# Performance work log

Measured on AMD Instinct MI355X. Metric: run time of the kernel, lower is better.

## Reference

```python
import jax, jax.numpy as jnp
import numpy as np

B, T, S, C, F = 32, 50, 2048, 8, 32  # batch, time, spatial steps, in-channels, filters
K, STRIDE = 2, 2
DN = ('NWC', 'WIO', 'NWC')


def hard_sigmoid(x):
    # TF-Keras hard_sigmoid: clip(0.2*x + 0.5, 0, 1)
    return jnp.clip(0.2 * x + 0.5, 0.0, 1.0)


def setup_inputs() -> dict:
    key = jax.random.key(0)
    ks = jax.random.split(key, 5)
    x = jax.random.normal(ks[0], (B, T, S, C), jnp.float32)
    kernel = jax.random.normal(ks[1], (K, C, 4 * F), jnp.float32) * 0.05
    rec_kernel = jax.random.normal(ks[2], (K, F, 4 * F), jnp.float32) * 0.05
    bias = jnp.zeros((4 * F,), jnp.float32)
    dense_w = jax.random.normal(ks[3], ((S // STRIDE) * F, 1), jnp.float32) * 0.02
    dense_b = jnp.zeros((1,), jnp.float32)
    return dict(x=x, kernel=kernel, rec_kernel=rec_kernel, bias=bias,
                dense_w=dense_w, dense_b=dense_b)


def reference(x, kernel, rec_kernel, bias, dense_w, dense_b):
    b, t, s, c = x.shape
    f = rec_kernel.shape[1]
    # Input convolution for all timesteps at once (stride 2, SAME padding)
    xc = jax.lax.conv_general_dilated(x.reshape(b * t, s, c), kernel,
                                      (STRIDE,), 'SAME', dimension_numbers=DN)
    xc = xc + bias
    sh = xc.shape[1]  # ceil(s / stride)
    xc = xc.reshape(b, t, sh, 4 * f).transpose(1, 0, 2, 3)  # time-major for scan

    def step(carry, xt):
        h, cst = carry
        hc = jax.lax.conv_general_dilated(h, rec_kernel, (1,), 'SAME',
                                          dimension_numbers=DN)
        z = xt + hc
        zi, zf, zc, zo = jnp.split(z, 4, axis=-1)
        i = hard_sigmoid(zi)
        fg = hard_sigmoid(zf)
        cst = fg * cst + i * jnp.tanh(zc)
        o = hard_sigmoid(zo)
        h = o * jnp.tanh(cst)
        return (h, cst), None

    h0 = jnp.zeros((b, sh, f), x.dtype)
    (h, _), _ = jax.lax.scan(step, (h0, h0), xc)
    # Flatten + Dense(1)
    return h.reshape(b, -1) @ dense_w + dense_b
```

## Files before the change

kernel.cpp:

```cpp
#include <hip/hip_runtime.h>


#define TT 50
#define LTILE 64
#define ROWS 129
#define HSTR 40

typedef __attribute__((ext_vector_type(8))) short short8;
typedef __attribute__((ext_vector_type(4))) float floatx4;

__device__ short8 g_tw0[512];
__device__ short8 g_tw1[512];
__device__ short8 g_txw[512];

__device__ __forceinline__ unsigned short f2b_rne(float f) {
  union { float f; unsigned u; } v; v.f = f;
  unsigned r = v.u + 0x7FFFu + ((v.u >> 16) & 1u);
  return (unsigned short)(r >> 16);
}
__device__ __forceinline__ unsigned short f2b_trunc(float f) {
  union { float f; unsigned u; } v; v.f = f;
  return (unsigned short)(v.u >> 16);
}
__device__ __forceinline__ float hsig(float x) {
  return __builtin_amdgcn_fmed3f(__builtin_fmaf(0.2f, x, 0.5f), 0.0f, 1.0f);
}
__device__ __forceinline__ float ftanh(float x) {
  float e = __expf(2.0f * x);
  return 1.0f - 2.0f * __builtin_amdgcn_rcpf(e + 1.0f);
}

__global__ void prep(const float* __restrict__ ks,
                     const float* __restrict__ rks,
                     const float* __restrict__ bs,
                     float* __restrict__ ws) {
  const int lane = threadIdx.x;
  if (lane < 32) ws[lane] = 0.0f;
  const int q  = lane >> 4;
  const int f0 = lane & 15;
#pragma unroll
  for (int n = 0; n < 8; ++n) {
    const int oc = (n >> 1) * 32 + 2 * f0 + (n & 1);
    short8 th;
#pragma unroll
    for (int j = 0; j < 8; ++j)
      th[j] = (short)f2b_rne(rks[(q * 8 + j) * 128 + oc]);
    g_tw0[n * 64 + lane] = th;
#pragma unroll
    for (int j = 0; j < 8; ++j)
      th[j] = (short)f2b_rne(rks[(32 + q * 8 + j) * 128 + oc]);
    g_tw1[n * 64 + lane] = th;
    short8 tx = {0, 0, 0, 0, 0, 0, 0, 0};
    if (q < 2) {
#pragma unroll
      for (int j = 0; j < 8; ++j)
        tx[j] = (short)f2b_rne(ks[(q * 8 + j) * 128 + oc]);
    } else if (q == 2) {
      tx[0] = (short)f2b_rne(bs[oc]);
    }
    g_txw[n * 64 + lane] = tx;
  }
}

__global__ __launch_bounds__(256, 2)
void convlstm_scan(const float* __restrict__ xs,
                   const float* __restrict__ dws,
                   float* __restrict__ acc_out) {
  __shared__ short hbH[2][ROWS * HSTR];

  const int tid  = threadIdx.x;
  const int b    = blockIdx.x >> 4;
  const int j0   = (blockIdx.x & 15) * LTILE;
  const int wave = tid >> 6;
  const int lane = tid & 63;
  const int q    = lane >> 4;
  const int f0   = lane & 15;

  for (int e = tid; e < ROWS * HSTR; e += 256)
    ((int*)hbH)[e] = 0;

  short8 Bwh0[8], Bwh1[8], Bxw[8];
#pragma unroll
  for (int n = 0; n < 8; ++n) {
    Bwh0[n] = g_tw0[n * 64 + lane];
    Bwh1[n] = g_tw1[n * 64 + lane];
    Bxw[n]  = g_txw[n * 64 + lane];
  }

  short8 axc = {0, 0, 0, 0, 0, 0, 0, 0};
  if (q == 2) axc[0] = (short)0x3F80;

  const floatx4 zero4 = {0.0f, 0.0f, 0.0f, 0.0f};

  float cst[2][8];
#pragma unroll
  for (int s = 0; s < 2; ++s)
#pragma unroll
    for (int i = 0; i < 8; ++i) cst[s][i] = 0.0f;

  floatx4 px0[2], px1[2];
#pragma unroll
  for (int s = 0; s < 2; ++s) {
    const int jr = (wave + 4 * s) * 16 + f0;
    const int jm = min(j0 + jr, 1023);
    const float* xp = xs + (size_t)b * TT * (2048 * 8) +
                      (size_t)(2 * jm + (q & 1)) * 8;
    px0[s] = *(const floatx4*)xp;
    px1[s] = *(const floatx4*)(xp + 4);
  }

  const int maxrows = 1024 - j0;
  float part = 0.0f;
  __syncthreads();

  for (int t = 0; t < TT; ++t) {
    const short* curH = hbH[t & 1];
    short* nxtH = hbH[(t & 1) ^ 1];
    int rows = LTILE + (TT - 1) - t;
    if (rows > maxrows) rows = maxrows;
    const int nmt = (rows + 15) >> 4;
    const int act1 = (wave + 4) < nmt;
    const int last = (t == TT - 1);
    const int tn = last ? t : t + 1;
    const float* xnext = xs + ((size_t)(b * TT + tn)) * (2048 * 8);

    short8 a0h[2], a1h[2];
#pragma unroll
    for (int s = 0; s < 2; ++s) {
      const int jr = (wave + 4 * s) * 16 + f0;
      a0h[s] = *(const short8*)&curH[jr * HSTR + q * 8];
      a1h[s] = *(const short8*)&curH[(jr + 1) * HSTR + q * 8];
    }

    short8 ax[2];
#pragma unroll
    for (int s = 0; s < 2; ++s) {
      ax[s] = axc;
      if (q < 2) {
        floatx4 x0 = px0[s], x1 = px1[s];
#pragma unroll
        for (int jj = 0; jj < 4; ++jj) ax[s][jj] = (short)f2b_trunc(x0[jj]);
#pragma unroll
        for (int jj = 0; jj < 4; ++jj) ax[s][4 + jj] = (short)f2b_trunc(x1[jj]);
      }
    }

#pragma unroll
    for (int s = 0; s < 2; ++s) {
      const int jr = (wave + 4 * s) * 16 + f0;
      const int jm = min(j0 + jr, 1023);
      const float* xp = xnext + (size_t)(2 * jm + (q & 1)) * 8;
      px0[s] = *(const floatx4*)xp;
      px1[s] = *(const floatx4*)(xp + 4);
    }

#pragma unroll
    for (int s = 0; s < 2; ++s) {
      if (s == 1 && !act1) continue;
      const int m = wave + 4 * s;

      floatx4 acc[8];
#pragma unroll
      for (int n = 0; n < 8; ++n)
        acc[n] = __builtin_amdgcn_mfma_f32_16x16x32_bf16(ax[s], Bxw[n], zero4, 0, 0, 0);
#pragma unroll
      for (int n = 0; n < 8; ++n)
        acc[n] = __builtin_amdgcn_mfma_f32_16x16x32_bf16(a0h[s], Bwh0[n], acc[n], 0, 0, 0);
#pragma unroll
      for (int n = 0; n < 8; ++n)
        acc[n] = __builtin_amdgcn_mfma_f32_16x16x32_bf16(a1h[s], Bwh1[n], acc[n], 0, 0, 0);

      const int jw = m * 16 + q * 4;
#pragma unroll
      for (int r = 0; r < 4; ++r) {
        float hv2[2];
#pragma unroll
        for (int p = 0; p < 2; ++p) {
          float zi = acc[0 + p][r], zf = acc[2 + p][r];
          float zc = acc[4 + p][r], zo = acc[6 + p][r];
          float ig = hsig(zi), fg = hsig(zf), og = hsig(zo);
          float cs = cst[s][p * 4 + r];
          float cn = __builtin_fmaf(fg, cs, ig * ftanh(zc));
          cst[s][p * 4 + r] = cn;
          hv2[p] = og * ftanh(cn);
        }
        if (!last) {
          unsigned pk;
          asm("v_cvt_pk_bf16_f32 %0, %1, %2"
              : "=v"(pk) : "v"(hv2[0]), "v"(hv2[1]));
          *(unsigned*)&nxtH[(jw + r) * HSTR + 2 * f0] = pk;
        } else {
          const int di = (j0 + jw + r) * 32 + 2 * f0;
          part = __builtin_fmaf(hv2[0], dws[di],
                 __builtin_fmaf(hv2[1], dws[di + 1], part));
        }
      }
    }
    __syncthreads();
  }

#pragma unroll
  for (int off = 32; off > 0; off >>= 1) part += __shfl_down(part, off);
  if (lane == 0) atomicAdd(&acc_out[b], part);
}

__global__ void finalize(const float* __restrict__ ws,
                         const float* __restrict__ db,
                         float* __restrict__ out) {
  int i = threadIdx.x;
  if (i < 32) out[i] = ws[i] + db[0];
}

extern "C" void kernel_launch(void* const* d_in, const int* in_sizes, int n_in,
                              void* d_out, int out_size, void* d_ws, size_t ws_size,
                              hipStream_t stream) {
  const float* x  = (const float*)d_in[0];
  const float* k  = (const float*)d_in[1];
  const float* rk = (const float*)d_in[2];
  const float* bi = (const float*)d_in[3];
  const float* dw = (const float*)d_in[4];
  const float* db = (const float*)d_in[5];
  float* ws = (float*)d_ws;
  float* out = (float*)d_out;

  hipLaunchKernelGGL(prep, dim3(1), dim3(64), 0, stream, k, rk, bi, ws);
  hipLaunchKernelGGL(convlstm_scan, dim3(512), dim3(256), 0, stream,
                     x, dw, ws);
  hipLaunchKernelGGL(finalize, dim3(1), dim3(64), 0, stream, ws, db, out);
}
```

Baseline: 233.4 us.

## Parallelize prep, rotate wave tiles, pack bf16 with perm, skip redundant loads

Prep now runs on 512 threads, one output tile per wave, instead of a single 64-thread loop. In the scan kernel, wave-to-tile assignment is rotated per block so the tail-tile work falls on different waves across blocks. Lanes with q>=2 no longer load x, since their loaded data was unused, and inactive second tiles skip their h loads. The bf16 truncation now packs pairs with v_perm, and tanh uses exp2 directly. Together these trim instruction count, memory traffic and wave load imbalance.

Result: slower. 254.8 us (+9.2%).

```diff
diff --git a/kernel.cpp b/kernel.cpp
--- a/kernel.cpp
+++ b/kernel.cpp
@@ -18,15 +18,11 @@
   unsigned r = v.u + 0x7FFFu + ((v.u >> 16) & 1u);
   return (unsigned short)(r >> 16);
 }
-__device__ __forceinline__ unsigned short f2b_trunc(float f) {
-  union { float f; unsigned u; } v; v.f = f;
-  return (unsigned short)(v.u >> 16);
-}
 __device__ __forceinline__ float hsig(float x) {
   return __builtin_amdgcn_fmed3f(__builtin_fmaf(0.2f, x, 0.5f), 0.0f, 1.0f);
 }
 __device__ __forceinline__ float ftanh(float x) {
-  float e = __expf(2.0f * x);
+  float e = __builtin_amdgcn_exp2f(x * 2.88539008177792681472f);
   return 1.0f - 2.0f * __builtin_amdgcn_rcpf(e + 1.0f);
 }
 
@@ -34,32 +30,32 @@
                      const float* __restrict__ rks,
                      const float* __restrict__ bs,
                      float* __restrict__ ws) {
-  const int lane = threadIdx.x;
-  if (lane < 32) ws[lane] = 0.0f;
-  const int q  = lane >> 4;
-  const int f0 = lane & 15;
-#pragma unroll
-  for (int n = 0; n < 8; ++n) {
-    const int oc = (n >> 1) * 32 + 2 * f0 + (n & 1);
-    short8 th;
+  const int tid  = threadIdx.x;
+  const int n    = tid >> 6;
+  const int lane = tid & 63;
+  const int q    = lane >> 4;
+  const int f0   = lane & 15;
+  if (tid < 32) ws[tid] = 0.0f;
+
+  const int oc = (n >> 1) * 32 + 2 * f0 + (n & 1);
+  short8 th;
+#pragma unroll
+  for (int j = 0; j < 8; ++j)
+    th[j] = (short)f2b_rne(rks[(q * 8 + j) * 128 + oc]);
+  g_tw0[n * 64 + lane] = th;
+#pragma unroll
+  for (int j = 0; j < 8; ++j)
+    th[j] = (short)f2b_rne(rks[(32 + q * 8 + j) * 128 + oc]);
+  g_tw1[n * 64 + lane] = th;
+  short8 tx = {0, 0, 0, 0, 0, 0, 0, 0};
+  if (q < 2) {
 #pragma unroll
     for (int j = 0; j < 8; ++j)
-      th[j] = (short)f2b_rne(rks[(q * 8 + j) * 128 + oc]);
-    g_tw0[n * 64 + lane] = th;
-#pragma unroll
-    for (int j = 0; j < 8; ++j)
-      th[j] = (short)f2b_rne(rks[(32 + q * 8 + j) * 128 + oc]);
-    g_tw1[n * 64 + lane] = th;
-    short8 tx = {0, 0, 0, 0, 0, 0, 0, 0};
-    if (q < 2) {
-#pragma unroll
-      for (int j = 0; j < 8; ++j)
-        tx[j] = (short)f2b_rne(ks[(q * 8 + j) * 128 + oc]);
-    } else if (q == 2) {
-      tx[0] = (short)f2b_rne(bs[oc]);
-    }
-    g_txw[n * 64 + lane] = tx;
-  }
+      tx[j] = (short)f2b_rne(ks[(q * 8 + j) * 128 + oc]);
+  } else if (q == 2) {
+    tx[0] = (short)f2b_rne(bs[oc]);
+  }
+  g_txw[n * 64 + lane] = tx;
 }
 
 __global__ __launch_bounds__(256, 2)
@@ -75,6 +71,8 @@
   const int lane = tid & 63;
   const int q    = lane >> 4;
   const int f0   = lane & 15;
+  const int rot  = 2 * ((blockIdx.x ^ (blockIdx.x >> 8)) & 1);
+  const int mrot = (wave + rot) & 3;
 
   for (int e = tid; e < ROWS * HSTR; e += 256)
     ((int*)hbH)[e] = 0;
@@ -101,12 +99,15 @@
   floatx4 px0[2], px1[2];
 #pragma unroll
   for (int s = 0; s < 2; ++s) {
-    const int jr = (wave + 4 * s) * 16 + f0;
+    px0[s] = zero4; px1[s] = zero4;
+    const int jr = (mrot + 4 * s) * 16 + f0;
     const int jm = min(j0 + jr, 1023);
-    const float* xp = xs + (size_t)b * TT * (2048 * 8) +
-                      (size_t)(2 * jm + (q & 1)) * 8;
-    px0[s] = *(const floatx4*)xp;
-    px1[s] = *(const floatx4*)(xp + 4);
+    if (q < 2) {
+      const float* xp = xs + (size_t)b * TT * (2048 * 8) +
+                        (size_t)(2 * jm + q) * 8;
+      px0[s] = *(const floatx4*)xp;
+      px1[s] = *(const floatx4*)(xp + 4);
+    }
   }
 
   const int maxrows = 1024 - j0;
@@ -119,7 +120,7 @@
     int rows = LTILE + (TT - 1) - t;
     if (rows > maxrows) rows = maxrows;
     const int nmt = (rows + 15) >> 4;
-    const int act1 = (wave + 4) < nmt;
+    const int act1 = (mrot + 4) < nmt;
     const int last = (t == TT - 1);
     const int tn = last ? t : t + 1;
     const float* xnext = xs + ((size_t)(b * TT + tn)) * (2048 * 8);
@@ -127,7 +128,8 @@
     short8 a0h[2], a1h[2];
 #pragma unroll
     for (int s = 0; s < 2; ++s) {
-      const int jr = (wave + 4 * s) * 16 + f0;
+      if (s == 1 && !act1) continue;
+      const int jr = (mrot + 4 * s) * 16 + f0;
       a0h[s] = *(const short8*)&curH[jr * HSTR + q * 8];
       a1h[s] = *(const short8*)&curH[(jr + 1) * HSTR + q * 8];
     }
@@ -137,19 +139,24 @@
     for (int s = 0; s < 2; ++s) {
       ax[s] = axc;
       if (q < 2) {
-        floatx4 x0 = px0[s], x1 = px1[s];
-#pragma unroll
-        for (int jj = 0; jj < 4; ++jj) ax[s][jj] = (short)f2b_trunc(x0[jj]);
-#pragma unroll
-        for (int jj = 0; jj < 4; ++jj) ax[s][4 + jj] = (short)f2b_trunc(x1[jj]);
+        unsigned* axw = (unsigned*)&ax[s];
+        axw[0] = __builtin_amdgcn_perm(__float_as_uint(px0[s][1]),
+                                       __float_as_uint(px0[s][0]), 0x07060302u);
+        axw[1] = __builtin_amdgcn_perm(__float_as_uint(px0[s][3]),
+                                       __float_as_uint(px0[s][2]), 0x07060302u);
+        axw[2] = __builtin_amdgcn_perm(__float_as_uint(px1[s][1]),
+                                       __float_as_uint(px1[s][0]), 0x07060302u);
+        axw[3] = __builtin_amdgcn_perm(__float_as_uint(px1[s][3]),
+                                       __float_as_uint(px1[s][2]), 0x07060302u);
       }
     }
 
 #pragma unroll
     for (int s = 0; s < 2; ++s) {
-      const int jr = (wave + 4 * s) * 16 + f0;
+      if (q >= 2) continue;
+      const int jr = (mrot + 4 * s) * 16 + f0;
       const int jm = min(j0 + jr, 1023);
-      const float* xp = xnext + (size_t)(2 * jm + (q & 1)) * 8;
+      const float* xp = xnext + (size_t)(2 * jm + q) * 8;
       px0[s] = *(const floatx4*)xp;
       px1[s] = *(const floatx4*)(xp + 4);
     }
@@ -157,7 +164,7 @@
 #pragma unroll
     for (int s = 0; s < 2; ++s) {
       if (s == 1 && !act1) continue;
-      const int m = wave + 4 * s;
+      const int m = mrot + 4 * s;
 
       floatx4 acc[8];
 #pragma unroll
@@ -223,7 +230,7 @@
   float* ws = (float*)d_ws;
   float* out = (float*)d_out;
 
-  hipLaunchKernelGGL(prep, dim3(1), dim3(64), 0, stream, k, rk, bi, ws);
+  hipLaunchKernelGGL(prep, dim3(1), dim3(512), 0, stream, k, rk, bi, ws);
   hipLaunchKernelGGL(convlstm_scan, dim3(512), dim3(256), 0, stream,
                      x, dw, ws);
   hipLaunchKernelGGL(finalize, dim3(1), dim3(64), 0, stream, ws, db, out);
```
